# Kernel tuning notes

Hardware: AMD Instinct MI355X
Metric: run time of the kernel (lower is better)

Reference implementation:

```python
import jax, jax.numpy as jnp
import numpy as np

ROPE_BASE = 10000.0

def _rope(x, positions):
    # x: (B, h, T, d); standard half-split rotary embedding with d_key = d
    d = x.shape[-1]
    inv_freq = 1.0 / (ROPE_BASE ** (jnp.arange(0, d // 2, dtype=jnp.float32) / (d // 2)))
    ang = positions.astype(jnp.float32)[:, None] * inv_freq[None, :]  # (T, d/2)
    cos, sin = jnp.cos(ang), jnp.sin(ang)
    x1, x2 = x[..., : d // 2], x[..., d // 2 :]
    return jnp.concatenate([x1 * cos - x2 * sin, x1 * sin + x2 * cos], axis=-1)


def setup_inputs() -> dict:
    key = jax.random.key(0)
    k1, k2, k3 = jax.random.split(key, 3)
    B, T, d, h = 2, 2048, 768, 8
    std = d ** -0.5
    x = jax.random.normal(k1, (B, T, d), dtype=jnp.float32)
    M = jax.random.normal(k2, (d, h * d), dtype=jnp.float32) * std
    V = jax.random.normal(k3, (d, h * d), dtype=jnp.float32) * std
    positions = jnp.arange(T, dtype=jnp.int32)
    return {"x": x, "M": M, "V": V, "positions": positions}


def reference(x, M, V, positions):
    B, T, d = x.shape
    h = M.shape[1] // d
    scale = 1.0 / jnp.sqrt(jnp.float32(d))
    # Q = RoPE(X @ M), K = RoPE(X) broadcast across heads, val = X @ V
    Q = (x @ M).reshape(B, T, h, d).transpose(0, 2, 1, 3)   # (B,h,T,d)
    val = (x @ V).reshape(B, T, h, d).transpose(0, 2, 1, 3)  # (B,h,T,d)
    K = jnp.broadcast_to(x[:, None, :, :], (B, h, T, d))     # (B,h,T,d)
    Q = _rope(Q, positions)
    K = _rope(K, positions)
    scores = jnp.einsum("bhqd,bhkd->bhqk", Q, K) * scale     # (B,h,T,T)
    causal = jnp.tril(jnp.ones((T, T), dtype=bool))          # True = keep
    scores = jnp.where(causal[None, None], scores, -jnp.inf)
    attn = jax.nn.softmax(scores, axis=-1)
    out = jnp.einsum("bhqk,bhkd->bhqd", attn, val)
    return out.sum(axis=1)  # sum over heads -> (B,T,d)
```

## Files before the change

### kernel.cpp

```cpp
#include <hip/hip_runtime.h>
#include <hip/hip_bf16.h>

typedef __bf16 bf16x8 __attribute__((ext_vector_type(8)));
typedef float f32x4 __attribute__((ext_vector_type(4)));

#define SCALE 0.03608439182435161f
#define NEGINF (-1e30f)

static __device__ __forceinline__ ushort f2bf(float f) {
    union { float f; unsigned u; } v; v.f = f;
    unsigned r = (v.u + 0x7fff + ((v.u >> 16) & 1)) >> 16;
    return (ushort)r;
}
static __device__ __forceinline__ float bf2f(ushort u) {
    union { unsigned u; float f; } v; v.u = ((unsigned)u) << 16;
    return v.f;
}

static __device__ __forceinline__ void gload16(const void* g, void* lds) {
    __builtin_amdgcn_global_load_lds((const __attribute__((address_space(1))) void*)g,
                                     (__attribute__((address_space(3))) void*)lds, 16, 0, 0);
}

#define BARV1 do { asm volatile("s_waitcnt vmcnt(1)" ::: "memory"); \
                   __builtin_amdgcn_s_barrier(); \
                   asm volatile("" ::: "memory"); } while (0)
#define BARV0 do { asm volatile("s_waitcnt vmcnt(0)" ::: "memory"); \
                   __builtin_amdgcn_s_barrier(); \
                   asm volatile("" ::: "memory"); } while (0)
#define BARL  do { asm volatile("s_waitcnt lgkmcnt(0)" ::: "memory"); \
                   __builtin_amdgcn_s_barrier(); \
                   asm volatile("" ::: "memory"); } while (0)

__global__ void k_convx(const float* __restrict__ x, ushort* __restrict__ xb, int n4) {
    int i = blockIdx.x * blockDim.x + threadIdx.x;
    if (i >= n4) return;
    float4 v = ((const float4*)x)[i];
    ushort4 o; o.x = f2bf(v.x); o.y = f2bf(v.y); o.z = f2bf(v.z); o.w = f2bf(v.w);
    ((ushort4*)xb)[i] = o;
}

__global__ void k_tconv(const float* __restrict__ in, ushort* __restrict__ out, int R, int C) {
    __shared__ float ts[32][33];
    int r0 = blockIdx.x * 32, c0 = blockIdx.y * 32;
    int lr = threadIdx.x >> 5, lc = threadIdx.x & 31;
#pragma unroll
    for (int i = 0; i < 4; i++) ts[lr + i * 8][lc] = in[(r0 + lr + i * 8) * C + c0 + lc];
    __syncthreads();
#pragma unroll
    for (int i = 0; i < 4; i++) out[(c0 + lr + i * 8) * R + r0 + lc] = f2bf(ts[lc][lr + i * 8]);
}

template <int EPI>
__global__ __launch_bounds__(256) void k_gemm(const ushort* __restrict__ A,
                                              const ushort* __restrict__ Bt,
                                              ushort* __restrict__ out) {
    __shared__ ushort As[128 * 40];
    __shared__ ushort Bs[128 * 40];
    const int m0 = blockIdx.x * 128, n0 = blockIdx.y * 128;
    const int tid = threadIdx.x, lane = tid & 63, wid = tid >> 6;
    const int wm = (wid >> 1) * 64, wn = (wid & 1) * 64;
    f32x4 acc[4][4] = {};

    for (int kt = 0; kt < 768; kt += 32) {
#pragma unroll
        for (int i = 0; i < 2; i++) {
            int c = tid + i * 256;
            int row = c >> 2, kc = (c & 3) * 8;
            uint4 va = *(const uint4*)&A[(m0 + row) * 768 + kt + kc];
            *(uint4*)&As[row * 40 + kc] = va;
            uint4 vb = *(const uint4*)&Bt[(n0 + row) * 768 + kt + kc];
            *(uint4*)&Bs[row * 40 + kc] = vb;
        }
        __syncthreads();
        bf16x8 af[4], bfr[4];
#pragma unroll
        for (int m = 0; m < 4; m++)
            af[m] = *(const bf16x8*)&As[(wm + m * 16 + (lane & 15)) * 40 + (lane >> 4) * 8];
#pragma unroll
        for (int n = 0; n < 4; n++)
            bfr[n] = *(const bf16x8*)&Bs[(wn + n * 16 + (lane & 15)) * 40 + (lane >> 4) * 8];
#pragma unroll
        for (int m = 0; m < 4; m++)
#pragma unroll
            for (int n = 0; n < 4; n++)
                acc[m][n] = __builtin_amdgcn_mfma_f32_16x16x32_bf16(af[m], bfr[n], acc[m][n], 0, 0, 0);
        __syncthreads();
    }

#pragma unroll
    for (int m = 0; m < 4; m++) {
#pragma unroll
        for (int n = 0; n < 4; n++) {
#pragma unroll
            for (int r = 0; r < 4; r++) {
                int row = m0 + wm + m * 16 + (lane >> 4) * 4 + r;
                int col = n0 + wn + n * 16 + (lane & 15);
                float v = acc[m][n][r];
                int idx;
                if (EPI == 0) {
                    int b = row >> 11, t = row & 2047;
                    int hh = col / 768, dd = col - hh * 768;
                    idx = ((b * 8 + hh) * 2048 + t) * 768 + dd;
                } else {
                    int hh = row / 768, dd = row - hh * 768;
                    int b = col >> 11, t = col & 2047;
                    idx = ((b * 8 + hh) * 768 + dd) * 2048 + t;
                }
                out[idx] = f2bf(v);
            }
        }
    }
}

__global__ void k_ropeq(ushort* __restrict__ Q, const int* __restrict__ pos, int nrows) {
    int i = blockIdx.x * blockDim.x + threadIdx.x;
    int row = i / 96, j4 = (i % 96) * 4;
    if (row >= nrows) return;
    float p = (float)pos[row & 2047];
    ushort4 u1 = *(ushort4*)&Q[row * 768 + j4];
    ushort4 u2 = *(ushort4*)&Q[row * 768 + 384 + j4];
    ushort4 o1, o2;
#pragma unroll
    for (int k = 0; k < 4; k++) {
        float inv = exp2f(-(float)(j4 + k) * (13.287712379549449f / 384.0f));
        float ang = p * inv;
        float s, c; sincosf(ang, &s, &c);
        float x1 = bf2f(((ushort*)&u1)[k]), x2 = bf2f(((ushort*)&u2)[k]);
        ((ushort*)&o1)[k] = f2bf((x1 * c - x2 * s) * SCALE);
        ((ushort*)&o2)[k] = f2bf((x1 * s + x2 * c) * SCALE);
    }
    *(ushort4*)&Q[row * 768 + j4] = o1;
    *(ushort4*)&Q[row * 768 + 384 + j4] = o2;
}

__global__ void k_ropek(const float* __restrict__ x, ushort* __restrict__ Kr,
                        const int* __restrict__ pos, int nrows) {
    int i = blockIdx.x * blockDim.x + threadIdx.x;
    int row = i / 96, j4 = (i % 96) * 4;
    if (row >= nrows) return;
    float p = (float)pos[row & 2047];
    float4 x1 = *(const float4*)&x[row * 768 + j4];
    float4 x2 = *(const float4*)&x[row * 768 + 384 + j4];
    ushort4 o1, o2;
    float a1[4] = {x1.x, x1.y, x1.z, x1.w};
    float a2[4] = {x2.x, x2.y, x2.z, x2.w};
#pragma unroll
    for (int k = 0; k < 4; k++) {
        float inv = exp2f(-(float)(j4 + k) * (13.287712379549449f / 384.0f));
        float ang = p * inv;
        float s, c; sincosf(ang, &s, &c);
        ((ushort*)&o1)[k] = f2bf(a1[k] * c - a2[k] * s);
        ((ushort*)&o2)[k] = f2bf(a1[k] * s + a2[k] * c);
    }
    *(ushort4*)&Kr[row * 768 + j4] = o1;
    *(ushort4*)&Kr[row * 768 + 384 + j4] = o2;
}

__global__ __launch_bounds__(1024, 4) void k_attn(const ushort* Qr, const ushort* __restrict__ Kr,
                                                  const ushort* __restrict__ valT, ushort* Oh) {
    __shared__ ushort Qs[6 * 8192];
    __shared__ ushort Buf[3][8192];
    __shared__ ushort SP[64 * 72];
    __shared__ float  resc_s[64], l_s[64];

    const int p = blockIdx.x, hh = blockIdx.y, b = blockIdx.z;
    const int bh = b * 8 + hh;
    const int tid = threadIdx.x, lane = tid & 63, wid = tid >> 6;
    const int wr = wid >> 2, wc = wid & 3;
    const int l15 = lane & 15, l4 = lane >> 4;
    const int srow = tid >> 4, slg = tid & 15;

    const int krow = tid >> 4;
    const int koff = ((tid & 15) * 16) ^ ((krow & 7) << 4);
    const int vrow = tid >> 3;
    const int voff = ((tid & 7) * 16) ^ ((vrow & 7) << 4);

    const char* Kptr = (const char*)Kr + (size_t)b * 2048 * 1536 + (size_t)krow * 1536 + koff;
    const char* Vptr = (const char*)valT + ((size_t)bh * 768 + vrow) * 4096 + voff;

    const int ra = wr * 16 + l15, rb_ = wc * 16 + l15;
    const int sa = (ra & 7) << 4, sb = (rb_ & 7) << 4;

    for (int ti = 0; ti < 2; ti++) {
        const int qt = ti ? (31 - p) : p;
        const int q0 = qt * 64;

        const char* qp = (const char*)Qr + ((size_t)(bh * 2048 + q0 + krow)) * 1536 + koff;
#pragma unroll
        for (int c = 0; c < 6; c++)
            gload16(qp + c * 256, Qs + c * 8192 + wid * 512);
        gload16(Kptr, Buf[0] + wid * 512);
        gload16(Kptr + 256, Buf[1] + wid * 512);

        float m_r = NEGINF, l_r = 0.f;
        f32x4 oacc[6][2] = {};

        for (int kb = 0; kb <= qt; kb++) {
            const char* kpc = Kptr + (size_t)kb * 98304;
            const char* vpc = Vptr + (size_t)kb * 128;
            const char* kpn = kpc + 98304;

            f32x4 s = {};
#pragma unroll
            for (int c = 0; c < 6; c++) {
                BARV1;
                if (c < 4)       gload16(kpc + (c + 2) * 256, Buf[(c + 2) % 3] + wid * 512);
                else if (c == 4) gload16(vpc,                 Buf[0] + wid * 512);
                else             gload16(vpc + 524288,        Buf[1] + wid * 512);
                const char* qc  = (const char*)Qs + c * 16384;
                const char* kcb = (const char*)Buf[c % 3];
                __builtin_amdgcn_s_setprio(1);
#pragma unroll
                for (int ks = 0; ks < 4; ks++) {
                    int kbyte = ks * 64 + l4 * 16;
                    bf16x8 a  = *(const bf16x8*)(qc  + ra  * 256 + (kbyte ^ sa));
                    bf16x8 bb = *(const bf16x8*)(kcb + rb_ * 256 + (kbyte ^ sb));
                    s = __builtin_amdgcn_mfma_f32_16x16x32_bf16(a, bb, s, 0, 0, 0);
                }
                __builtin_amdgcn_s_setprio(0);
            }

#pragma unroll
            for (int r = 0; r < 4; r++)
                *(ushort*)((char*)SP + (wr * 16 + l4 * 4 + r) * 144 + (wc * 16 + l15) * 2) = f2bf(s[r]);
            BARL;

            {
                uint2 sw = *(const uint2*)((const char*)SP + srow * 144 + slg * 8);
                float vv[4];
                vv[0] = bf2f((ushort)(sw.x & 0xffffu));
                vv[1] = bf2f((ushort)(sw.x >> 16));
                vv[2] = bf2f((ushort)(sw.y & 0xffffu));
                vv[3] = bf2f((ushort)(sw.y >> 16));
                if (kb == qt) {
                    const int grow = q0 + srow, cb = kb * 64 + slg * 4;
#pragma unroll
                    for (int j = 0; j < 4; j++) if (cb + j > grow) vv[j] = NEGINF;
                }
                float pmax = fmaxf(fmaxf(vv[0], vv[1]), fmaxf(vv[2], vv[3]));
#pragma unroll
                for (int m2 = 1; m2 < 16; m2 <<= 1) pmax = fmaxf(pmax, __shfl_xor(pmax, m2));
                float m_new = fmaxf(m_r, pmax);
                float rv = __expf(m_r - m_new);
                float psum = 0.f; ushort pb[4];
#pragma unroll
                for (int j = 0; j < 4; j++) {
                    float pp = __expf(vv[j] - m_new);
                    psum += pp; pb[j] = f2bf(pp);
                }
#pragma unroll
                for (int m2 = 1; m2 < 16; m2 <<= 1) psum += __shfl_xor(psum, m2);
                l_r = l_r * rv + psum; m_r = m_new;
                uint2 pw; pw.x = pb[0] | ((uint)pb[1] << 16); pw.y = pb[2] | ((uint)pb[3] << 16);
                *(uint2*)((char*)SP + srow * 144 + slg * 8) = pw;
                if (slg == 0) resc_s[srow] = rv;
            }
            BARL;

            float4 rf = *(const float4*)&resc_s[wr * 16 + l4 * 4];
            const float* rfp = (const float*)&rf;
#pragma unroll
            for (int c = 0; c < 6; c++)
#pragma unroll
                for (int n = 0; n < 2; n++)
#pragma unroll
                    for (int r = 0; r < 4; r++) oacc[c][n][r] *= rfp[r];
            bf16x8 pa0 = *(const bf16x8*)((const char*)SP + (wr * 16 + l15) * 144 + l4 * 16);
            bf16x8 pa1 = *(const bf16x8*)((const char*)SP + (wr * 16 + l15) * 144 + 64 + l4 * 16);

#pragma unroll
            for (int c = 0; c < 6; c++) {
                if (c < 5) { BARV1; }
                else if (kb < qt) { BARV1; }
                else { BARV0; }
                if (c < 4) gload16(vpc + (size_t)(c + 2) * 524288, Buf[(c + 2) % 3] + wid * 512);
                else if (kb < qt) {
                    if (c == 4) gload16(kpn,       Buf[0] + wid * 512);
                    else        gload16(kpn + 256, Buf[1] + wid * 512);
                }
                const char* vcb = (const char*)Buf[c % 3];
                __builtin_amdgcn_s_setprio(1);
#pragma unroll
                for (int kc2 = 0; kc2 < 2; kc2++) {
                    bf16x8 a = kc2 ? pa1 : pa0;
#pragma unroll
                    for (int n = 0; n < 2; n++) {
                        int rvr = wc * 32 + n * 16 + l15;
                        bf16x8 bb = *(const bf16x8*)(vcb + rvr * 128 + ((kc2 * 64 + l4 * 16) ^ ((rvr & 7) << 4)));
                        oacc[c][n] = __builtin_amdgcn_mfma_f32_16x16x32_bf16(a, bb, oacc[c][n], 0, 0, 0);
                    }
                }
                __builtin_amdgcn_s_setprio(0);
            }
        }

        if (slg == 0) l_s[srow] = l_r;
        BARL;
        float4 lf = *(const float4*)&l_s[wr * 16 + l4 * 4];
        const float* lfp = (const float*)&lf;
        float inv_[4];
#pragma unroll
        for (int r = 0; r < 4; r++) inv_[r] = 1.0f / lfp[r];
        ushort* orow = Oh + (size_t)(bh * 2048 + q0) * 768;
#pragma unroll
        for (int c = 0; c < 6; c++)
#pragma unroll
            for (int n = 0; n < 2; n++) {
                int dd = c * 128 + wc * 32 + n * 16 + l15;
#pragma unroll
                for (int r = 0; r < 4; r++)
                    orow[(size_t)(wr * 16 + l4 * 4 + r) * 768 + dd] = f2bf(oacc[c][n][r] * inv_[r]);
            }
    }
}

__global__ void k_reduce(const ushort* __restrict__ Oh, float* __restrict__ out) {
    int i = blockIdx.x * blockDim.x + threadIdx.x;
    if (i >= 786432) return;
    size_t base = (size_t)i * 4;
    int b = (base >= 1572864) ? 1 : 0;
    size_t rem = base - (size_t)b * 1572864;
    const ushort* src = Oh + (size_t)b * 8 * 1572864 + rem;
    float4 acc = {0.f, 0.f, 0.f, 0.f};
#pragma unroll
    for (int h = 0; h < 8; h++) {
        ushort4 v = *(const ushort4*)(src + (size_t)h * 1572864);
        acc.x += bf2f(v.x); acc.y += bf2f(v.y); acc.z += bf2f(v.z); acc.w += bf2f(v.w);
    }
    *(float4*)&out[base] = acc;
}

extern "C" void kernel_launch(void* const* d_in, const int* in_sizes, int n_in,
                              void* d_out, int out_size, void* d_ws, size_t ws_size,
                              hipStream_t stream) {
    const float* x = (const float*)d_in[0];
    const float* M = (const float*)d_in[1];
    const float* V = (const float*)d_in[2];
    const int* pos = (const int*)d_in[3];
    float* out = (float*)d_out;
    char* ws = (char*)d_ws;

    ushort* xb   = (ushort*)(ws);
    ushort* Mt   = (ushort*)(ws + 6291456);
    ushort* Vt   = (ushort*)(ws + 15728640);
    ushort* Qr   = (ushort*)(ws + 25165824);
    ushort* valT = (ushort*)(ws + 75497472);
    ushort* Kr   = (ushort*)(ws + 125829120);

    k_convx<<<3072, 256, 0, stream>>>(x, xb, 786432);
    k_tconv<<<dim3(24, 192), 256, 0, stream>>>(M, Mt, 768, 6144);
    k_tconv<<<dim3(24, 192), 256, 0, stream>>>(V, Vt, 768, 6144);
    k_gemm<0><<<dim3(32, 48), 256, 0, stream>>>(xb, Mt, Qr);
    k_gemm<1><<<dim3(48, 32), 256, 0, stream>>>(Vt, xb, valT);
    k_ropeq<<<12288, 256, 0, stream>>>(Qr, pos, 32768);
    k_ropek<<<1536, 256, 0, stream>>>(x, Kr, pos, 4096);
    k_attn<<<dim3(16, 8, 2), 1024, 0, stream>>>(Qr, Kr, valT, Qr );
    k_reduce<<<3072, 256, 0, stream>>>(Qr, out);
}
```

Baseline: 404.7 us.

## Restructure attention kernel with 128-wide key tiles and 32x32 MFMA

```diff
diff --git a/kernel.cpp b/kernel.cpp
--- a/kernel.cpp
+++ b/kernel.cpp
@@ -3,6 +3,7 @@
 
 typedef __bf16 bf16x8 __attribute__((ext_vector_type(8)));
 typedef float f32x4 __attribute__((ext_vector_type(4)));
+typedef float f32x16 __attribute__((ext_vector_type(16)));
 
 #define SCALE 0.03608439182435161f
 #define NEGINF (-1e30f)
@@ -22,15 +23,12 @@
                                      (__attribute__((address_space(3))) void*)lds, 16, 0, 0);
 }
 
-#define BARV1 do { asm volatile("s_waitcnt vmcnt(1)" ::: "memory"); \
-                   __builtin_amdgcn_s_barrier(); \
-                   asm volatile("" ::: "memory"); } while (0)
-#define BARV0 do { asm volatile("s_waitcnt vmcnt(0)" ::: "memory"); \
-                   __builtin_amdgcn_s_barrier(); \
-                   asm volatile("" ::: "memory"); } while (0)
-#define BARL  do { asm volatile("s_waitcnt lgkmcnt(0)" ::: "memory"); \
-                   __builtin_amdgcn_s_barrier(); \
-                   asm volatile("" ::: "memory"); } while (0)
+#define PHASE_SYNC do { asm volatile("s_waitcnt vmcnt(0) lgkmcnt(0)" ::: "memory"); \
+                        __builtin_amdgcn_s_barrier(); \
+                        asm volatile("" ::: "memory"); } while (0)
+#define BARL do { asm volatile("s_waitcnt lgkmcnt(0)" ::: "memory"); \
+                  __builtin_amdgcn_s_barrier(); \
+                  asm volatile("" ::: "memory"); } while (0)
 
 __global__ void k_convx(const float* __restrict__ x, ushort* __restrict__ xb, int n4) {
     int i = blockIdx.x * blockDim.x + threadIdx.x;
@@ -157,161 +155,178 @@
     *(ushort4*)&Kr[row * 768 + 384 + j4] = o2;
 }
 
-__global__ __launch_bounds__(1024, 4) void k_attn(const ushort* Qr, const ushort* __restrict__ Kr,
-                                                  const ushort* __restrict__ valT, ushort* Oh) {
-    __shared__ ushort Qs[6 * 8192];
-    __shared__ ushort Buf[3][8192];
-    __shared__ ushort SP[64 * 72];
-    __shared__ float  resc_s[64], l_s[64];
+__global__ __launch_bounds__(512, 2) void k_attn(const ushort* Qr, const ushort* __restrict__ Kr,
+                                                 const ushort* __restrict__ valT, ushort* Oh) {
+    __shared__ alignas(128) char Qs[98304];
+    __shared__ alignas(128) char pool[65536];
 
     const int p = blockIdx.x, hh = blockIdx.y, b = blockIdx.z;
     const int bh = b * 8 + hh;
     const int tid = threadIdx.x, lane = tid & 63, wid = tid >> 6;
-    const int wr = wid >> 2, wc = wid & 3;
-    const int l15 = lane & 15, l4 = lane >> 4;
-    const int srow = tid >> 4, slg = tid & 15;
-
-    const int krow = tid >> 4;
-    const int koff = ((tid & 15) * 16) ^ ((krow & 7) << 4);
-    const int vrow = tid >> 3;
-    const int voff = ((tid & 7) * 16) ^ ((vrow & 7) << 4);
-
-    const char* Kptr = (const char*)Kr + (size_t)b * 2048 * 1536 + (size_t)krow * 1536 + koff;
-    const char* Vptr = (const char*)valT + ((size_t)bh * 768 + vrow) * 4096 + voff;
-
-    const int ra = wr * 16 + l15, rb_ = wc * 16 + l15;
-    const int sa = (ra & 7) << 4, sb = (rb_ & 7) << 4;
+    const int g = wid & 3, qh = wid >> 2;
+    const int l31 = lane & 31, hi = lane >> 5;
+    const int hi16 = hi << 4;
+
+    const int row0 = tid >> 4, col16 = tid & 15;
+    const int swz = (col16 << 4) ^ ((row0 & 15) << 4);
+
+    const int arow = g * 32 + l31;
+    const int qrow = qh * 32 + l31;
+    const int asw = (arow & 15) << 4;
+    const int qsw = (qrow & 15) << 4;
+
+    char* Pb = pool + 32768;
+    float* pmax_s = (float*)(pool + 49152);
+    float* psum_s = (float*)(pool + 50176);
+    float* stat_s = (float*)(pool + 51200);
+
+    const char* Kb0 = (const char*)Kr + ((size_t)(b * 2048 + row0)) * 1536 + swz;
+    const char* Vb0 = (const char*)valT + ((size_t)(bh * 768 + row0)) * 4096 + swz;
 
     for (int ti = 0; ti < 2; ti++) {
         const int qt = ti ? (31 - p) : p;
         const int q0 = qt * 64;
-
-        const char* qp = (const char*)Qr + ((size_t)(bh * 2048 + q0 + krow)) * 1536 + koff;
-#pragma unroll
-        for (int c = 0; c < 6; c++)
-            gload16(qp + c * 256, Qs + c * 8192 + wid * 512);
-        gload16(Kptr, Buf[0] + wid * 512);
-        gload16(Kptr + 256, Buf[1] + wid * 512);
+        const int nkb = (qt + 2) >> 1;
+        const int qg = q0 + qrow;
+
+        const char* qsrc = (const char*)Qr + ((size_t)(bh * 2048 + q0 + row0)) * 1536 + swz;
+#pragma unroll
+        for (int r = 0; r < 12; r++)
+            gload16(qsrc + (r >> 1) * 256 + (size_t)(r & 1) * 49152,
+                    Qs + (r >> 1) * 16384 + (r & 1) * 8192 + wid * 1024);
+#pragma unroll
+        for (int r = 0; r < 4; r++)
+            gload16(Kb0 + (size_t)r * 49152, pool + r * 8192 + wid * 1024);
 
         float m_r = NEGINF, l_r = 0.f;
-        f32x4 oacc[6][2] = {};
-
-        for (int kb = 0; kb <= qt; kb++) {
-            const char* kpc = Kptr + (size_t)kb * 98304;
-            const char* vpc = Vptr + (size_t)kb * 128;
-            const char* kpn = kpc + 98304;
-
-            f32x4 s = {};
+        f32x16 oacc[6] = {};
+
+        for (int kb = 0; kb < nkb; kb++) {
+            const char* kc = Kb0 + (size_t)kb * 196608;
+            const char* vc = Vb0 + (size_t)kb * 256;
+
+            f32x16 sacc = {};
 #pragma unroll
             for (int c = 0; c < 6; c++) {
-                BARV1;
-                if (c < 4)       gload16(kpc + (c + 2) * 256, Buf[(c + 2) % 3] + wid * 512);
-                else if (c == 4) gload16(vpc,                 Buf[0] + wid * 512);
-                else             gload16(vpc + 524288,        Buf[1] + wid * 512);
-                const char* qc  = (const char*)Qs + c * 16384;
-                const char* kcb = (const char*)Buf[c % 3];
+                PHASE_SYNC;
+                if (c < 5) {
+#pragma unroll
+                    for (int r = 0; r < 4; r++)
+                        gload16(kc + (c + 1) * 256 + (size_t)r * 49152,
+                                pool + ((c + 1) & 1) * 32768 + r * 8192 + wid * 1024);
+                } else {
+#pragma unroll
+                    for (int r = 0; r < 4; r++)
+                        gload16(vc + (size_t)r * 131072, pool + r * 8192 + wid * 1024);
+                }
+                const char* kbuf = pool + (c & 1) * 32768;
+                const char* qcb = Qs + c * 16384;
                 __builtin_amdgcn_s_setprio(1);
 #pragma unroll
-                for (int ks = 0; ks < 4; ks++) {
-                    int kbyte = ks * 64 + l4 * 16;
-                    bf16x8 a  = *(const bf16x8*)(qc  + ra  * 256 + (kbyte ^ sa));
-                    bf16x8 bb = *(const bf16x8*)(kcb + rb_ * 256 + (kbyte ^ sb));
-                    s = __builtin_amdgcn_mfma_f32_16x16x32_bf16(a, bb, s, 0, 0, 0);
+                for (int s = 0; s < 8; s++) {
+                    bf16x8 a = *(const bf16x8*)(kbuf + arow * 256 + ((s * 32 + hi16) ^ asw));
+                    bf16x8 bq = *(const bf16x8*)(qcb + qrow * 256 + ((s * 32 + hi16) ^ qsw));
+                    sacc = __builtin_amdgcn_mfma_f32_32x32x16_bf16(a, bq, sacc, 0, 0, 0);
                 }
                 __builtin_amdgcn_s_setprio(0);
             }
 
-#pragma unroll
-            for (int r = 0; r < 4; r++)
-                *(ushort*)((char*)SP + (wr * 16 + l4 * 4 + r) * 144 + (wc * 16 + l15) * 2) = f2bf(s[r]);
+            __builtin_amdgcn_s_barrier();
+
+            const int kbase_ = kb * 128 + g * 32 + 4 * hi;
+            float mloc = NEGINF;
+#pragma unroll
+            for (int r = 0; r < 16; r++) {
+                int kg = kbase_ + (r & 3) + 8 * (r >> 2);
+                float v = (kg > qg) ? NEGINF : sacc[r];
+                mloc = fmaxf(mloc, v);
+            }
+            mloc = fmaxf(mloc, __shfl_xor(mloc, 32));
+            if (hi == 0) pmax_s[qrow * 4 + g] = mloc;
             BARL;
 
-            {
-                uint2 sw = *(const uint2*)((const char*)SP + srow * 144 + slg * 8);
-                float vv[4];
-                vv[0] = bf2f((ushort)(sw.x & 0xffffu));
-                vv[1] = bf2f((ushort)(sw.x >> 16));
-                vv[2] = bf2f((ushort)(sw.y & 0xffffu));
-                vv[3] = bf2f((ushort)(sw.y >> 16));
-                if (kb == qt) {
-                    const int grow = q0 + srow, cb = kb * 64 + slg * 4;
-#pragma unroll
-                    for (int j = 0; j < 4; j++) if (cb + j > grow) vv[j] = NEGINF;
-                }
-                float pmax = fmaxf(fmaxf(vv[0], vv[1]), fmaxf(vv[2], vv[3]));
-#pragma unroll
-                for (int m2 = 1; m2 < 16; m2 <<= 1) pmax = fmaxf(pmax, __shfl_xor(pmax, m2));
-                float m_new = fmaxf(m_r, pmax);
-                float rv = __expf(m_r - m_new);
-                float psum = 0.f; ushort pb[4];
-#pragma unroll
-                for (int j = 0; j < 4; j++) {
-                    float pp = __expf(vv[j] - m_new);
-                    psum += pp; pb[j] = f2bf(pp);
-                }
-#pragma unroll
-                for (int m2 = 1; m2 < 16; m2 <<= 1) psum += __shfl_xor(psum, m2);
-                l_r = l_r * rv + psum; m_r = m_new;
-                uint2 pw; pw.x = pb[0] | ((uint)pb[1] << 16); pw.y = pb[2] | ((uint)pb[3] << 16);
-                *(uint2*)((char*)SP + srow * 144 + slg * 8) = pw;
-                if (slg == 0) resc_s[srow] = rv;
+            float4 pm = *(const float4*)&pmax_s[qrow * 4];
+            float m_new = fmaxf(fmaxf(fmaxf(pm.x, pm.y), fmaxf(pm.z, pm.w)), m_r);
+            float rv = __expf(m_r - m_new);
+            float ps = 0.f; uint w[8];
+#pragma unroll
+            for (int j = 0; j < 8; j++) {
+                int kg0 = kbase_ + ((2 * j) & 3) + 8 * ((2 * j) >> 2);
+                int kg1 = kbase_ + ((2 * j + 1) & 3) + 8 * ((2 * j + 1) >> 2);
+                float e0 = (kg0 > qg) ? 0.f : __expf(sacc[2 * j] - m_new);
+                float e1 = (kg1 > qg) ? 0.f : __expf(sacc[2 * j + 1] - m_new);
+                ps += e0 + e1;
+                w[j] = (uint)f2bf(e0) | ((uint)f2bf(e1) << 16);
+            }
+            ps += __shfl_xor(ps, 32);
+            if (hi == 0) psum_s[qrow * 4 + g] = ps;
+            if (g == 0 && hi == 0) stat_s[qrow] = rv;
+#pragma unroll
+            for (int j = 0; j < 4; j++) {
+                uint2 pw; pw.x = w[2 * j]; pw.y = w[2 * j + 1];
+                *(uint2*)(Pb + qrow * 256 + ((g * 64 + j * 16 + hi * 8) ^ qsw)) = pw;
             }
             BARL;
 
-            float4 rf = *(const float4*)&resc_s[wr * 16 + l4 * 4];
-            const float* rfp = (const float*)&rf;
+            float4 ps4 = *(const float4*)&psum_s[qrow * 4];
+            l_r = l_r * rv + (ps4.x + ps4.y + ps4.z + ps4.w);
+            m_r = m_new;
+            float rs[16];
+#pragma unroll
+            for (int r = 0; r < 16; r++)
+                rs[r] = stat_s[qh * 32 + (r & 3) + 8 * (r >> 2) + 4 * hi];
 #pragma unroll
             for (int c = 0; c < 6; c++)
 #pragma unroll
-                for (int n = 0; n < 2; n++)
-#pragma unroll
-                    for (int r = 0; r < 4; r++) oacc[c][n][r] *= rfp[r];
-            bf16x8 pa0 = *(const bf16x8*)((const char*)SP + (wr * 16 + l15) * 144 + l4 * 16);
-            bf16x8 pa1 = *(const bf16x8*)((const char*)SP + (wr * 16 + l15) * 144 + 64 + l4 * 16);
+                for (int r = 0; r < 16; r++) oacc[c][r] *= rs[r];
+            bf16x8 pa[8];
+#pragma unroll
+            for (int s = 0; s < 8; s++)
+                pa[s] = *(const bf16x8*)(Pb + qrow * 256 + ((s * 32 + hi16) ^ qsw));
 
 #pragma unroll
             for (int c = 0; c < 6; c++) {
-                if (c < 5) { BARV1; }
-                else if (kb < qt) { BARV1; }
-                else { BARV0; }
-                if (c < 4) gload16(vpc + (size_t)(c + 2) * 524288, Buf[(c + 2) % 3] + wid * 512);
-                else if (kb < qt) {
-                    if (c == 4) gload16(kpn,       Buf[0] + wid * 512);
-                    else        gload16(kpn + 256, Buf[1] + wid * 512);
-                }
-                const char* vcb = (const char*)Buf[c % 3];
+                PHASE_SYNC;
+                if (c < 5) {
+#pragma unroll
+                    for (int r = 0; r < 4; r++)
+                        gload16(vc + (size_t)(c + 1) * 524288 + (size_t)r * 131072,
+                                pool + ((c + 1) & 1) * 32768 + r * 8192 + wid * 1024);
+                } else if (kb + 1 < nkb) {
+#pragma unroll
+                    for (int r = 0; r < 4; r++)
+                        gload16(kc + 196608 + (size_t)r * 49152, pool + r * 8192 + wid * 1024);
+                }
+                const char* vbuf = pool + (c & 1) * 32768;
                 __builtin_amdgcn_s_setprio(1);
 #pragma unroll
-                for (int kc2 = 0; kc2 < 2; kc2++) {
-                    bf16x8 a = kc2 ? pa1 : pa0;
-#pragma unroll
-                    for (int n = 0; n < 2; n++) {
-                        int rvr = wc * 32 + n * 16 + l15;
-                        bf16x8 bb = *(const bf16x8*)(vcb + rvr * 128 + ((kc2 * 64 + l4 * 16) ^ ((rvr & 7) << 4)));
-                        oacc[c][n] = __builtin_amdgcn_mfma_f32_16x16x32_bf16(a, bb, oacc[c][n], 0, 0, 0);
-                    }
+                for (int s = 0; s < 8; s++) {
+                    bf16x8 bv = *(const bf16x8*)(vbuf + arow * 256 + ((s * 32 + hi16) ^ asw));
+                    oacc[c] = __builtin_amdgcn_mfma_f32_32x32x16_bf16(pa[s], bv, oacc[c], 0, 0, 0);
                 }
                 __builtin_amdgcn_s_setprio(0);
             }
         }
 
-        if (slg == 0) l_s[srow] = l_r;
+        asm volatile("s_waitcnt vmcnt(0) lgkmcnt(0)" ::: "memory");
+        __builtin_amdgcn_s_barrier();
+        if (g == 0 && hi == 0) stat_s[qrow] = l_r;
         BARL;
-        float4 lf = *(const float4*)&l_s[wr * 16 + l4 * 4];
-        const float* lfp = (const float*)&lf;
-        float inv_[4];
-#pragma unroll
-        for (int r = 0; r < 4; r++) inv_[r] = 1.0f / lfp[r];
-        ushort* orow = Oh + (size_t)(bh * 2048 + q0) * 768;
-#pragma unroll
-        for (int c = 0; c < 6; c++)
-#pragma unroll
-            for (int n = 0; n < 2; n++) {
-                int dd = c * 128 + wc * 32 + n * 16 + l15;
-#pragma unroll
-                for (int r = 0; r < 4; r++)
-                    orow[(size_t)(wr * 16 + l4 * 4 + r) * 768 + dd] = f2bf(oacc[c][n][r] * inv_[r]);
-            }
+        float inv16[16];
+#pragma unroll
+        for (int r = 0; r < 16; r++)
+            inv16[r] = 1.0f / stat_s[qh * 32 + (r & 3) + 8 * (r >> 2) + 4 * hi];
+        BARL;
+        ushort* obase = Oh + ((size_t)(bh * 2048 + q0 + qh * 32)) * 768;
+#pragma unroll
+        for (int c = 0; c < 6; c++) {
+            int dd = c * 128 + g * 32 + l31;
+#pragma unroll
+            for (int r = 0; r < 16; r++) {
+                int rq = (r & 3) + 8 * (r >> 2) + 4 * hi;
+                obase[(size_t)rq * 768 + dd] = f2bf(oacc[c][r] * inv16[r]);
+            }
+        }
     }
 }
 
@@ -355,6 +370,6 @@
     k_gemm<1><<<dim3(48, 32), 256, 0, stream>>>(Vt, xb, valT);
     k_ropeq<<<12288, 256, 0, stream>>>(Qr, pos, 32768);
     k_ropek<<<1536, 256, 0, stream>>>(x, Kr, pos, 4096);
-    k_attn<<<dim3(16, 8, 2), 1024, 0, stream>>>(Qr, Kr, valT, Qr );
+    k_attn<<<dim3(16, 8, 2), 512, 0, stream>>>(Qr, Kr, valT, Qr );
     k_reduce<<<3072, 256, 0, stream>>>(Qr, out);
 }
```

New measurement: 371.6 us. 8.2% less time.
